# Optimization experiments

Hardware: AMD Instinct MI355X
Metric: run time of the kernel (lower is better)

Reference implementation:

```python
import jax, jax.numpy as jnp
import numpy as np
from jax import lax

N_FREE = 10
DT = 0.1
COMP = 4


def setup_inputs() -> dict:
    key = jax.random.key(0)
    kx, kw = jax.random.split(key)
    B, D = 256, 16384
    nodes = D // COMP  # 4096
    x = jax.random.normal(kx, (B, D), dtype=jnp.float32)
    # Hopfield-style node-coupling matrix (learned parameter), small init for stable relaxation
    W = jax.random.normal(kw, (nodes, nodes), dtype=jnp.float32) * 0.02
    return {"x": x, "W": W}


def reference(x, W):
    B, D = x.shape
    nodes = D // COMP
    # project scalar features to multivectors (B, nodes, comp)
    x_mv = x.reshape(B, nodes, COMP)
    W_sym = 0.5 * (W + W.T)  # symmetric coupling => well-defined energy

    def step(h, _):
        rho = jnp.tanh(h)                                      # (B, nodes, comp)
        drive = jnp.einsum('nm,bmc->bnc', W_sym, rho) + x_mv   # recurrent + input coupling
        grad_E = h - (1.0 - rho * rho) * drive                 # dE/dh
        return h - DT * grad_E, None

    h_free, _ = lax.scan(step, x_mv, None, length=N_FREE)
    return h_free[..., 0]  # scalar (grade-0) component, (B, nodes)
```

## Files before the change

### kernel.cpp

```cpp
#include <hip/hip_runtime.h>
#include <hip/hip_bf16.h>


#define NODES 4096
#define KDIM  4096
#define MDIM  1024
#define DLEN  16384
#define HALF_ELEMS 4194304

typedef __attribute__((ext_vector_type(8))) __bf16 bf16x8;
typedef __attribute__((ext_vector_type(8))) unsigned short u16x8;
typedef __attribute__((ext_vector_type(4))) float  f32x4;

static __device__ __forceinline__ unsigned short f32_to_bf16(float f) {
    unsigned int u = __float_as_uint(f);
    u += 0x7fffu + ((u >> 16) & 1u);
    return (unsigned short)(u >> 16);
}
static __device__ __forceinline__ float bf16_to_f32(unsigned short u) {
    return __uint_as_float(((unsigned int)u) << 16);
}

__global__ __launch_bounds__(256)
void symw_kernel(const float* __restrict__ W, unsigned short* __restrict__ Wbp) {
    __shared__ float Ta[64][64];
    __shared__ float Tb[64][65];
    const int tn = blockIdx.y, tm = blockIdx.x;
    const int c  = threadIdx.x & 63;
    const int r0 = threadIdx.x >> 6;
#pragma unroll
    for (int rr = 0; rr < 16; ++rr) {
        int r = r0 * 16 + rr;
        Ta[r][c] = W[(size_t)(tn * 64 + r) * 4096 + tm * 64 + c];
        Tb[r][c] = W[(size_t)(tm * 64 + r) * 4096 + tn * 64 + c];
    }
    __syncthreads();
#pragma unroll
    for (int rr = 0; rr < 16; ++rr) {
        int r = r0 * 16 + rr;
        float v = 0.5f * (Ta[r][c] + Tb[c][r]);
        int n = tn * 64 + r;
        int k = tm * 64 + c;
        size_t addr = ((size_t)(k >> 5) * 256 + (n >> 4)) * 512
                    + (size_t)((n & 15) | (((k >> 3) & 3) << 4)) * 8 + (k & 7);
        Wbp[addr] = f32_to_bf16(v);
    }
}

__global__ __launch_bounds__(256)
void init_kernel(const float* __restrict__ x, float* __restrict__ h,
                 unsigned short* __restrict__ P0) {
    int idx = blockIdx.x * blockDim.x + threadIdx.x;
    int b = idx >> 12;
    int m = idx & 4095;
    f32x4 xv = *(const f32x4*)(x + (size_t)idx * 4);
    *(f32x4*)(h + (size_t)idx * 4) = xv;
    size_t base = ((size_t)(m >> 5) * 64 + (b >> 2)) * 512
                + (size_t)((m >> 3) & 3) * 128 + (m & 7);
#pragma unroll
    for (int c = 0; c < 4; ++c) {
        P0[base + (size_t)((b & 3) * 4 + c) * 8] = f32_to_bf16(tanhf(xv[c]));
    }
}

__global__ __launch_bounds__(64, 2)
void gemm_kernel(const unsigned short* __restrict__ Pcur,
                 const unsigned short* __restrict__ Wbp,
                 unsigned short* __restrict__ Dp) {
    __shared__ unsigned short Bs[4 * 2048];

    const int lane = threadIdx.x;
    const int bx   = blockIdx.x;
    const int by   = blockIdx.y;
    const int ks   = blockIdx.z;
    const int T0   = ks * 64;

    size_t soff[4];
#pragma unroll
    for (int j = 0; j < 4; ++j)
        soff[j] = ((size_t)(bx * 4 + j)) * 512 + (size_t)lane * 8;
    size_t aoff[4];
#pragma unroll
    for (int mi = 0; mi < 4; ++mi)
        aoff[mi] = ((size_t)(by * 4 + mi)) * 512 + (size_t)lane * 8;

    f32x4 acc[4][4];
#pragma unroll
    for (int mi = 0; mi < 4; ++mi)
#pragma unroll
        for (int ni = 0; ni < 4; ++ni)
            acc[mi][ni] = (f32x4){0.f, 0.f, 0.f, 0.f};

    bf16x8 aA[4], aB[4];

#define TC(t) ((t) < 63 ? (t) : 63)

#define STAGE(slot, tl)                                                         \
    do {                                                                        \
        const unsigned short* src =                                             \
            Wbp + (size_t)(T0 + (tl)) * 131072;                                 \
        _Pragma("unroll")                                                       \
        for (int j = 0; j < 4; ++j) {                                           \
            __builtin_amdgcn_global_load_lds(                                   \
                (const __attribute__((address_space(1))) void*)(src + soff[j]), \
                (__attribute__((address_space(3))) void*)                      \
                    (Bs + (slot) * 2048 + j * 512 + lane * 8),                  \
                16, 0, 0);                                                      \
        }                                                                       \
    } while (0)

#define LOADA(s, tl)                                                            \
    do {                                                                        \
        const unsigned short* Pt = Pcur + (size_t)(T0 + (tl)) * 32768;          \
        _Pragma("unroll")                                                       \
        for (int mi = 0; mi < 4; ++mi)                                          \
            s[mi] = *(const bf16x8*)(Pt + aoff[mi]);                            \
    } while (0)

#define COMPUTE(slot, s)                                                        \
    do {                                                                        \
        const unsigned short* Bb = Bs + (slot) * 2048;                          \
        bf16x8 bfr[4];                                                          \
        _Pragma("unroll")                                                       \
        for (int ni = 0; ni < 4; ++ni)                                          \
            bfr[ni] = *(const bf16x8*)(Bb + ni * 512 + lane * 8);               \
        _Pragma("unroll")                                                       \
        for (int mi = 0; mi < 4; ++mi)                                          \
            _Pragma("unroll")                                                   \
            for (int ni = 0; ni < 4; ++ni)                                      \
                acc[mi][ni] = __builtin_amdgcn_mfma_f32_16x16x32_bf16(          \
                    s[mi], bfr[ni], acc[mi][ni], 0, 0, 0);                      \
    } while (0)

    STAGE(0, 0);
    LOADA(aA, 0);
    STAGE(1, 1);
    STAGE(2, 2);
    LOADA(aB, 1);
    STAGE(3, 3);
    asm volatile("s_waitcnt vmcnt(16)" ::: "memory");
    COMPUTE(0, aA);

    for (int tp = 0; tp < 31; ++tp) {
        const int t = 1 + 2 * tp;
        LOADA(aA, TC(t + 1));
        STAGE((t + 3) & 3, TC(t + 3));
        asm volatile("s_waitcnt vmcnt(12)" ::: "memory");
        COMPUTE(t & 3, aB);

        const int u = t + 1;
        LOADA(aB, TC(u + 1));
        STAGE((u + 3) & 3, TC(u + 3));
        asm volatile("s_waitcnt vmcnt(12)" ::: "memory");
        COMPUTE(u & 3, aA);
    }
    asm volatile("s_waitcnt vmcnt(0)" ::: "memory");
    COMPUTE(3, aB);
#undef STAGE
#undef LOADA
#undef COMPUTE
#undef TC

    const int lr = lane & 15, lk = lane >> 4;
    unsigned short* D = Dp + (size_t)ks * HALF_ELEMS;
#pragma unroll
    for (int mi = 0; mi < 4; ++mi) {
        int i0 = by * 64 + mi * 16 + lk * 4;
#pragma unroll
        for (int ni = 0; ni < 4; ++ni) {
            int n = bx * 64 + ni * 16 + lr;
#pragma unroll
            for (int r = 0; r < 4; ++r)
                D[(size_t)(i0 + r) * NODES + n] = f32_to_bf16(acc[mi][ni][r]);
        }
    }
}

__global__ __launch_bounds__(256)
void combine_kernel(const unsigned short* __restrict__ Dp,
                    const float* __restrict__ x,
                    float* __restrict__ h,
                    unsigned short* __restrict__ Pnxt,
                    float* __restrict__ out) {
    int g  = blockIdx.x * 256 + threadIdx.x;
    int b  = g >> 9;
    int mg = (g & 511) << 3;
    size_t hbase = (size_t)b * DLEN + (size_t)mg * 4;

    f32x4 hv[8], xv[8];
#pragma unroll
    for (int e = 0; e < 8; ++e) {
        hv[e] = *(const f32x4*)(h + hbase + e * 4);
        xv[e] = *(const f32x4*)(x + hbase + e * 4);
    }
    u16x8 d0[4], d1[4];
#pragma unroll
    for (int c = 0; c < 4; ++c) {
        d0[c] = *(const u16x8*)(Dp + (size_t)(b * 4 + c) * NODES + mg);
        d1[c] = *(const u16x8*)(Dp + HALF_ELEMS + (size_t)(b * 4 + c) * NODES + mg);
    }
    u16x8 pn[4];
    float o[8];
#pragma unroll
    for (int e = 0; e < 8; ++e) {
#pragma unroll
        for (int c = 0; c < 4; ++c) {
            float p    = bf16_to_f32(d0[c][e]) + bf16_to_f32(d1[c][e]);
            float hvv  = hv[e][c];
            float rho  = tanhf(hvv);
            float drive = p + xv[e][c];
            float hnew = 0.9f * hvv + 0.1f * (1.0f - rho * rho) * drive;
            hv[e][c] = hnew;
            pn[c][e] = f32_to_bf16(tanhf(hnew));
            if (c == 0) o[e] = hnew;
        }
    }
#pragma unroll
    for (int e = 0; e < 8; ++e)
        *(f32x4*)(h + hbase + e * 4) = hv[e];
#pragma unroll
    for (int c = 0; c < 4; ++c) {
        size_t pa = (size_t)(mg >> 5) * 32768 + (size_t)(b >> 2) * 512
                  + (size_t)(((b & 3) * 4 + c) | (((mg >> 3) & 3) << 4)) * 8;
        *(u16x8*)(Pnxt + pa) = pn[c];
    }
    if (out) {
        *(f32x4*)(out + (size_t)b * NODES + mg)     = (f32x4){o[0], o[1], o[2], o[3]};
        *(f32x4*)(out + (size_t)b * NODES + mg + 4) = (f32x4){o[4], o[5], o[6], o[7]};
    }
}

extern "C" void kernel_launch(void* const* d_in, const int* in_sizes, int n_in,
                              void* d_out, int out_size, void* d_ws, size_t ws_size,
                              hipStream_t stream) {
    const float* x = (const float*)d_in[0];
    const float* W = (const float*)d_in[1];
    float* out = (float*)d_out;

    char* ws = (char*)d_ws;
    unsigned short* Wbp = (unsigned short*)(ws);
    unsigned short* P0  = (unsigned short*)(ws + ((size_t)32 << 20));
    unsigned short* P1  = (unsigned short*)(ws + ((size_t)40 << 20));
    float*          h   = (float*)(ws + ((size_t)48 << 20));
    unsigned short* Dp  = (unsigned short*)(ws + ((size_t)64 << 20));

    symw_kernel<<<dim3(64, 64), 256, 0, stream>>>(W, Wbp);
    init_kernel<<<dim3(4096), 256, 0, stream>>>(x, h, P0);

    unsigned short* pc = P0;
    unsigned short* pn = P1;
    for (int s = 0; s < 10; ++s) {
        gemm_kernel<<<dim3(64, 16, 2), 64, 0, stream>>>(pc, Wbp, Dp);
        combine_kernel<<<dim3(512), 256, 0, stream>>>(
            Dp, x, h, pn, (s == 9) ? out : nullptr);
        unsigned short* t = pc; pc = pn; pn = t;
    }
}
```

Measured before the change: 653.9 us.

## Enlarge GEMM tile to 128x128 with four waves sharing LDS-staged W

```diff
diff --git a/kernel.cpp b/kernel.cpp
--- a/kernel.cpp
+++ b/kernel.cpp
@@ -63,26 +63,36 @@
     }
 }
 
-__global__ __launch_bounds__(64, 2)
+__global__ __launch_bounds__(256, 2)
 void gemm_kernel(const unsigned short* __restrict__ Pcur,
                  const unsigned short* __restrict__ Wbp,
                  unsigned short* __restrict__ Dp) {
-    __shared__ unsigned short Bs[4 * 2048];
-
-    const int lane = threadIdx.x;
-    const int bx   = blockIdx.x;
-    const int by   = blockIdx.y;
-    const int ks   = blockIdx.z;
+    __shared__ unsigned short Bs[4 * 4096];
+
+    const int id   = blockIdx.x;
+    const int bx   = (id & 7) * 4 + ((id >> 3) & 3);
+    const int by   = (id >> 5) & 7;
+    const int ks   = id >> 8;
     const int T0   = ks * 64;
 
-    size_t soff[4];
-#pragma unroll
-    for (int j = 0; j < 4; ++j)
-        soff[j] = ((size_t)(bx * 4 + j)) * 512 + (size_t)lane * 8;
+    const int tid  = threadIdx.x;
+    const int w    = tid >> 6;
+    const int lane = tid & 63;
+    const int wm   = w >> 1;
+    const int wn   = w & 1;
+
+    size_t soff[2]; int dsto[2];
+#pragma unroll
+    for (int j = 0; j < 2; ++j) {
+        int c = tid + 256 * j;
+        soff[j] = ((size_t)(bx * 8 + (c >> 6))) * 512 + (size_t)(c & 63) * 8;
+        dsto[j] = c * 8;
+    }
     size_t aoff[4];
 #pragma unroll
     for (int mi = 0; mi < 4; ++mi)
-        aoff[mi] = ((size_t)(by * 4 + mi)) * 512 + (size_t)lane * 8;
+        aoff[mi] = ((size_t)(by * 8 + wm * 4 + mi)) * 512 + (size_t)lane * 8;
+    const int boff = (wn * 4) * 512 + lane * 8;
 
     f32x4 acc[4][4];
 #pragma unroll
@@ -97,14 +107,13 @@
 
 #define STAGE(slot, tl)                                                         \
     do {                                                                        \
-        const unsigned short* src =                                             \
-            Wbp + (size_t)(T0 + (tl)) * 131072;                                 \
-        _Pragma("unroll")                                                       \
-        for (int j = 0; j < 4; ++j) {                                           \
+        const unsigned short* src = Wbp + (size_t)(T0 + (tl)) * 131072;         \
+        _Pragma("unroll")                                                       \
+        for (int j = 0; j < 2; ++j) {                                           \
             __builtin_amdgcn_global_load_lds(                                   \
                 (const __attribute__((address_space(1))) void*)(src + soff[j]), \
                 (__attribute__((address_space(3))) void*)                      \
-                    (Bs + (slot) * 2048 + j * 512 + lane * 8),                  \
+                    (Bs + (slot) * 4096 + dsto[j]),                             \
                 16, 0, 0);                                                      \
         }                                                                       \
     } while (0)
@@ -119,11 +128,11 @@
 
 #define COMPUTE(slot, s)                                                        \
     do {                                                                        \
-        const unsigned short* Bb = Bs + (slot) * 2048;                          \
+        const unsigned short* Bb = Bs + (slot) * 4096;                          \
         bf16x8 bfr[4];                                                          \
         _Pragma("unroll")                                                       \
         for (int ni = 0; ni < 4; ++ni)                                          \
-            bfr[ni] = *(const bf16x8*)(Bb + ni * 512 + lane * 8);               \
+            bfr[ni] = *(const bf16x8*)(Bb + boff + ni * 512);                   \
         _Pragma("unroll")                                                       \
         for (int mi = 0; mi < 4; ++mi)                                          \
             _Pragma("unroll")                                                   \
@@ -138,23 +147,27 @@
     STAGE(2, 2);
     LOADA(aB, 1);
     STAGE(3, 3);
-    asm volatile("s_waitcnt vmcnt(16)" ::: "memory");
+    asm volatile("s_waitcnt vmcnt(10)" ::: "memory");
+    __builtin_amdgcn_s_barrier();
     COMPUTE(0, aA);
 
     for (int tp = 0; tp < 31; ++tp) {
         const int t = 1 + 2 * tp;
         LOADA(aA, TC(t + 1));
         STAGE((t + 3) & 3, TC(t + 3));
-        asm volatile("s_waitcnt vmcnt(12)" ::: "memory");
+        asm volatile("s_waitcnt vmcnt(10)" ::: "memory");
+        __builtin_amdgcn_s_barrier();
         COMPUTE(t & 3, aB);
 
         const int u = t + 1;
         LOADA(aB, TC(u + 1));
         STAGE((u + 3) & 3, TC(u + 3));
-        asm volatile("s_waitcnt vmcnt(12)" ::: "memory");
+        asm volatile("s_waitcnt vmcnt(10)" ::: "memory");
+        __builtin_amdgcn_s_barrier();
         COMPUTE(u & 3, aA);
     }
     asm volatile("s_waitcnt vmcnt(0)" ::: "memory");
+    __builtin_amdgcn_s_barrier();
     COMPUTE(3, aB);
 #undef STAGE
 #undef LOADA
@@ -165,10 +178,10 @@
     unsigned short* D = Dp + (size_t)ks * HALF_ELEMS;
 #pragma unroll
     for (int mi = 0; mi < 4; ++mi) {
-        int i0 = by * 64 + mi * 16 + lk * 4;
+        int i0 = by * 128 + wm * 64 + mi * 16 + lk * 4;
 #pragma unroll
         for (int ni = 0; ni < 4; ++ni) {
-            int n = bx * 64 + ni * 16 + lr;
+            int n = bx * 128 + wn * 64 + ni * 16 + lr;
 #pragma unroll
             for (int r = 0; r < 4; ++r)
                 D[(size_t)(i0 + r) * NODES + n] = f32_to_bf16(acc[mi][ni][r]);
@@ -215,14 +228,16 @@
             if (c == 0) o[e] = hnew;
         }
     }
-#pragma unroll
-    for (int e = 0; e < 8; ++e)
-        *(f32x4*)(h + hbase + e * 4) = hv[e];
-#pragma unroll
-    for (int c = 0; c < 4; ++c) {
-        size_t pa = (size_t)(mg >> 5) * 32768 + (size_t)(b >> 2) * 512
-                  + (size_t)(((b & 3) * 4 + c) | (((mg >> 3) & 3) << 4)) * 8;
-        *(u16x8*)(Pnxt + pa) = pn[c];
+    if (Pnxt) {
+#pragma unroll
+        for (int e = 0; e < 8; ++e)
+            *(f32x4*)(h + hbase + e * 4) = hv[e];
+#pragma unroll
+        for (int c = 0; c < 4; ++c) {
+            size_t pa = (size_t)(mg >> 5) * 32768 + (size_t)(b >> 2) * 512
+                      + (size_t)(((b & 3) * 4 + c) | (((mg >> 3) & 3) << 4)) * 8;
+            *(u16x8*)(Pnxt + pa) = pn[c];
+        }
     }
     if (out) {
         *(f32x4*)(out + (size_t)b * NODES + mg)     = (f32x4){o[0], o[1], o[2], o[3]};
@@ -250,9 +265,9 @@
     unsigned short* pc = P0;
     unsigned short* pn = P1;
     for (int s = 0; s < 10; ++s) {
-        gemm_kernel<<<dim3(64, 16, 2), 64, 0, stream>>>(pc, Wbp, Dp);
+        gemm_kernel<<<dim3(512), 256, 0, stream>>>(pc, Wbp, Dp);
         combine_kernel<<<dim3(512), 256, 0, stream>>>(
-            Dp, x, h, pn, (s == 9) ? out : nullptr);
+            Dp, x, h, (s == 9) ? nullptr : pn, (s == 9) ? out : nullptr);
         unsigned short* t = pc; pc = pn; pn = t;
     }
 }
```

After: 586.7 us. -10.3%, faster.
